# Kernel tuning notes

Hardware: AMD Instinct MI355X
Metric: run time of the kernel (lower is better)

Reference implementation:

```python
import jax, jax.numpy as jnp
import numpy as np

# Fixed supermask = [3, 4, 16, 28, 0, 0, 0, 3]:
#   preproc: relu(Linear x3); l1 = GCN(x); l2 = GCN(l1); l3 = GCN(l2);
#   out = relu(Linear z3((l1+l2+l3)/3))
HIDDEN = 64


def gcn_conv(h, W, b, src, dst, norm, n_nodes):
    # PyG GCNConv: h' = scatter_add(norm * (hW)[src] -> dst) + b
    hw = h @ W                                  # [N, F]
    msg = hw[src] * norm[:, None]               # gather + scale  [E+N, F]
    agg = jax.ops.segment_sum(msg, dst, num_segments=n_nodes)
    return agg + b


def setup_inputs() -> dict:
    key = jax.random.key(0)
    ks = jax.random.split(key, 12)
    N, E, NFEAT, NCLASS = 100000, 1000000, 256, 40
    x = jax.random.normal(ks[0], (N, NFEAT), dtype=jnp.float32)
    edge_index = jax.random.randint(ks[1], (2, E), 0, N, dtype=jnp.int64)
    s = 1.0 / np.sqrt(NFEAT)
    h = 1.0 / np.sqrt(HIDDEN)
    return {
        "x": x,
        "edge_index": edge_index,
        "Wx": jax.random.uniform(ks[2], (NFEAT, HIDDEN), jnp.float32, -s, s),
        "bx": jnp.zeros((HIDDEN,), jnp.float32),
        "W1": jax.random.uniform(ks[3], (HIDDEN, HIDDEN), jnp.float32, -h, h),
        "b1": jnp.zeros((HIDDEN,), jnp.float32),
        "W2": jax.random.uniform(ks[4], (HIDDEN, HIDDEN), jnp.float32, -h, h),
        "b2": jnp.zeros((HIDDEN,), jnp.float32),
        "W3": jax.random.uniform(ks[5], (HIDDEN, HIDDEN), jnp.float32, -h, h),
        "b3": jnp.zeros((HIDDEN,), jnp.float32),
        "Wz": jax.random.uniform(ks[6], (HIDDEN, NCLASS), jnp.float32, -h, h),
        "bz": jnp.zeros((NCLASS,), jnp.float32),
    }


def reference(x, edge_index, Wx, bx, W1, b1, W2, b2, W3, b3, Wz, bz):
    n = x.shape[0]
    # add self-loops (PyG GCNConv default)
    loop = jnp.arange(n, dtype=edge_index.dtype)
    src = jnp.concatenate([edge_index[0], loop])
    dst = jnp.concatenate([edge_index[1], loop])
    deg = jax.ops.segment_sum(jnp.ones_like(dst, dtype=x.dtype), dst, num_segments=n)
    dinv = jnp.where(deg > 0, jax.lax.rsqrt(deg), 0.0)
    norm = dinv[src] * dinv[dst]                 # [E+N]

    h0 = jax.nn.relu(x @ Wx + bx)                # x_3(relu) o x3(Linear)
    l1 = gcn_conv(h0, W1, b1, src, dst, norm, n)
    l2 = gcn_conv(l1, W2, b2, src, dst, norm, n)
    l3 = gcn_conv(l2, W3, b3, src, dst, norm, n)
    z = (l1 + l2 + l3) / 3.0
    return jax.nn.relu(z @ Wz + bz)
```

## Files before the change

kernel.cpp:

```cpp
#include <hip/hip_runtime.h>

#define NFEAT 256
#define HID 64
#define NCLASS 40
#define EPB 4096
#define BCAP 8192

typedef _Float16 half8 __attribute__((ext_vector_type(8)));
typedef float floatx4 __attribute__((ext_vector_type(4)));

struct BinSM {
    int lcnt[256], loff[256], lcur[256], gbase[256], sc[256];
    int sdst[EPB];
    int words[EPB];
};

__global__ __launch_bounds__(256) void k_pre(const int* __restrict__ src, const int* __restrict__ dst,
                                             int* __restrict__ bcur, int* __restrict__ bwords,
                                             int nbuckets, int E, int nbin,
                                             const float* __restrict__ W1, const float* __restrict__ W2,
                                             const float* __restrict__ W3, _Float16* __restrict__ Wt16,
                                             const float* __restrict__ x, const float* __restrict__ Wx,
                                             const float* __restrict__ bx, _Float16* __restrict__ h0,
                                             int N, int ngemm) {
    __shared__ __align__(16) char smraw[sizeof(BinSM)];
    int t = threadIdx.x;
    int bid = blockIdx.x;

    if (bid >= nbin && bid < nbin + 3) {
        int l = bid - nbin;
        const float* Ws = (l == 0) ? W1 : (l == 1) ? W2 : W3;
        _Float16* wt = Wt16 + l * 4096;
        for (int i = t; i < 4096; i += 256) {
            int col = i >> 6, k = i & 63;
            wt[i] = (_Float16)Ws[k * HID + col];
        }
        return;
    }

    if (bid >= nbin + 3) {
        _Float16 (*Wt)[264] = (_Float16 (*)[264])smraw;
        {
            int c = t & 63, k0 = (t >> 6) * 64;
            for (int k = k0; k < k0 + 64; ++k)
                Wt[c][k] = (_Float16)Wx[k * HID + c];
        }
        __syncthreads();
        int lane = t & 63, wv = t >> 6;
        int lg = lane >> 4, ln = lane & 15;
        int gb = bid - nbin - 3;
        int wid = gb * 4 + wv;
        int nw = ngemm * 4;
        float bb[4];
        #pragma unroll
        for (int g = 0; g < 4; ++g) bb[g] = bx[g * 16 + ln];
        int ntiles = N >> 4;
        for (int tile = wid; tile < ntiles; tile += nw) {
            int row0 = tile << 4;
            const float* xr = x + (size_t)(row0 + ln) * NFEAT + lg * 8;
            float4 av[16];
            #pragma unroll
            for (int ks = 0; ks < 8; ++ks) {
                av[2 * ks]     = *(const float4*)(xr + ks * 32);
                av[2 * ks + 1] = *(const float4*)(xr + ks * 32 + 4);
            }
            floatx4 acc[4] = {{0.f,0.f,0.f,0.f},{0.f,0.f,0.f,0.f},{0.f,0.f,0.f,0.f},{0.f,0.f,0.f,0.f}};
            #pragma unroll
            for (int ks = 0; ks < 8; ++ks) {
                float4 a0 = av[2 * ks], a1 = av[2 * ks + 1];
                half8 a;
                a[0]=(_Float16)a0.x; a[1]=(_Float16)a0.y; a[2]=(_Float16)a0.z; a[3]=(_Float16)a0.w;
                a[4]=(_Float16)a1.x; a[5]=(_Float16)a1.y; a[6]=(_Float16)a1.z; a[7]=(_Float16)a1.w;
                #pragma unroll
                for (int g = 0; g < 4; ++g) {
                    half8 b = *(const half8*)&Wt[g * 16 + ln][ks * 32 + lg * 8];
                    acc[g] = __builtin_amdgcn_mfma_f32_16x16x32_f16(a, b, acc[g], 0, 0, 0);
                }
            }
            #pragma unroll
            for (int g = 0; g < 4; ++g) {
                #pragma unroll
                for (int r = 0; r < 4; ++r) {
                    int row = row0 + lg * 4 + r;
                    h0[(size_t)row * HID + g * 16 + ln] = (_Float16)fmaxf(acc[g][r] + bb[g], 0.f);
                }
            }
        }
        return;
    }

    BinSM* sm = (BinSM*)smraw;
    int base = bid * EPB;
    int n = E - base; if (n > EPB) n = EPB;
    sm->lcnt[t] = 0;
    __syncthreads();
    for (int i = t; i < n; i += 256) {
        int d = dst[base + i];
        sm->sdst[i] = d;
        atomicAdd(&sm->lcnt[d >> 9], 1);
    }
    __syncthreads();
    int v = sm->lcnt[t];
    sm->sc[t] = v; __syncthreads();
    for (int o = 1; o < 256; o <<= 1) {
        int add = (t >= o) ? sm->sc[t - o] : 0;
        __syncthreads();
        sm->sc[t] += add;
        __syncthreads();
    }
    int excl = sm->sc[t] - v;
    sm->loff[t] = excl; sm->lcur[t] = excl;
    __syncthreads();
    for (int i = t; i < n; i += 256) {
        int d = sm->sdst[i], s = src[base + i];
        int b = d >> 9;
        int p = atomicAdd(&sm->lcur[b], 1);
        sm->words[p] = s | ((d & 511) << 17);
    }
    __syncthreads();
    if (t < nbuckets) {
        int c = sm->lcnt[t];
        sm->gbase[t] = c > 0 ? atomicAdd(&bcur[t], c) : 0;
    }
    __syncthreads();
    int lane = t & 63, wv = t >> 6;
    for (int b = wv; b < nbuckets; b += 4) {
        int o = sm->loff[b], c = sm->lcnt[b], gb = sm->gbase[b];
        int* dstp = bwords + (size_t)b * BCAP;
        for (int i = lane; i < c; i += 64) {
            int gp = gb + i;
            if (gp < BCAP) dstp[gp] = sm->words[o + i];
        }
    }
}

__global__ __launch_bounds__(256) void k_csr(const int* __restrict__ bcur, const int* __restrict__ bwords,
                                             int* __restrict__ csr, unsigned* __restrict__ pk,
                                             float* __restrict__ dinv, int N) {
    __shared__ int cnt[512], cur[512], sc[256];
    __shared__ int lcsr[BCAP];
    int t = threadIdx.x;
    int b = blockIdx.x;
    int nodebase = b << 9;
    int nb = bcur[b]; if (nb > BCAP) nb = BCAP;
    cnt[t] = 0; cnt[t + 256] = 0;
    __syncthreads();
    const int* wp = bwords + (size_t)b * BCAP;
    for (int i = t; i < nb; i += 256)
        atomicAdd(&cnt[wp[i] >> 17], 1);
    __syncthreads();
    int v0 = cnt[2 * t], v1 = cnt[2 * t + 1];
    int p = v0 + v1;
    sc[t] = p; __syncthreads();
    for (int o = 1; o < 256; o <<= 1) {
        int add = (t >= o) ? sc[t - o] : 0;
        __syncthreads();
        sc[t] += add;
        __syncthreads();
    }
    int e = sc[t] - p;
    cur[2 * t] = e; cur[2 * t + 1] = e + v0;
    #pragma unroll
    for (int j = 0; j < 2; ++j) {
        int node = nodebase + 2 * t + j;
        if (node < N) {
            int c = cnt[2 * t + j]; if (c > 2047) c = 2047;
            pk[node] = (unsigned)(b * BCAP + cur[2 * t + j]) | ((unsigned)c << 21);
            dinv[node] = rsqrtf((float)c + 1.0f);
        }
    }
    __syncthreads();
    for (int i = t; i < nb; i += 256) {
        int w = wp[i];
        int pos = atomicAdd(&cur[w >> 17], 1);
        lcsr[pos] = w & 0x1FFFF;
    }
    __syncthreads();
    int* cp = csr + (size_t)b * BCAP;
    for (int i = t; i < nb; i += 256) cp[i] = lcsr[i];
}

template<int WRN>
__global__ __launch_bounds__(256) void k_layer(const _Float16* __restrict__ Ph, const int* __restrict__ csr,
                                               const unsigned* __restrict__ pk, const float* __restrict__ dinv,
                                               const _Float16* __restrict__ Wt, const float* __restrict__ b,
                                               float* __restrict__ normf,
                                               _Float16* __restrict__ Lout, int N) {
    __shared__ _Float16 z[32][72];
    __shared__ _Float16 ot[32][72];
    int t = threadIdx.x;
    int lane = t & 63, wv = t >> 6;
    int sg = lane >> 3, f8 = lane & 7;
    int lg = lane >> 4, ln = lane & 15;
    int nb = blockIdx.x << 5;
    int node = nb + wv * 8 + sg;
    bool valid = node < N;
    int nodec = valid ? node : (N - 1);
    int col = wv * 16 + ln;
    half8 bf0 = *(const half8*)(Wt + col * 64 + lg * 8);
    half8 bf1 = *(const half8*)(Wt + col * 64 + 32 + lg * 8);
    float bb = b[col];

    unsigned pkv = valid ? pk[node] : 0u;
    int off = (int)(pkv & 0x1FFFFFu);
    int c = (int)(pkv >> 21);
    float dd = valid ? dinv[node] : 0.f;
    const _Float16* pb = Ph + f8 * 8;
    float acc[8];
    {
        half8 self = *(const half8*)(pb + (size_t)nodec * HID);
        float dd2 = dd * dd;
        #pragma unroll
        for (int j = 0; j < 8; ++j) acc[j] = (float)self[j] * dd2;
    }
    int ecur = f8;
    bool ok = ecur < c;
    int s_cur = ok ? csr[off + ecur] : nodec;
    float nm_cur;
    if (WRN) {
        nm_cur = ok ? dinv[s_cur] * dd : 0.f;
        if (ok) normf[off + ecur] = nm_cur;
    } else {
        nm_cur = ok ? normf[off + ecur] : 0.f;
    }
    for (int jj = 0; jj < c; jj += 8) {
        int en = jj + 8 + f8;
        bool okn = en < c;
        int s_nxt = okn ? csr[off + en] : nodec;
        float nm_nxt;
        if (WRN) {
            nm_nxt = okn ? dinv[s_nxt] * dd : 0.f;
            if (okn) normf[off + en] = nm_nxt;
        } else {
            nm_nxt = okn ? normf[off + en] : 0.f;
        }
        #pragma unroll
        for (int j = 0; j < 8; ++j) {
            int ss = __shfl(s_cur, j, 8);
            float nn = __shfl(nm_cur, j, 8);
            half8 v = *(const half8*)(pb + (size_t)ss * HID);
            #pragma unroll
            for (int q = 0; q < 8; ++q) acc[q] = fmaf((float)v[q], nn, acc[q]);
        }
        s_cur = s_nxt; nm_cur = nm_nxt;
    }
    {
        half8 zv;
        #pragma unroll
        for (int j = 0; j < 8; ++j) zv[j] = (_Float16)acc[j];
        *(half8*)&z[wv * 8 + sg][f8 * 8] = zv;
    }
    __syncthreads();
    floatx4 acc0 = {0.f, 0.f, 0.f, 0.f}, acc1 = {0.f, 0.f, 0.f, 0.f};
    {
        half8 a0 = *(const half8*)&z[ln][lg * 8];
        half8 a1 = *(const half8*)&z[16 + ln][lg * 8];
        acc0 = __builtin_amdgcn_mfma_f32_16x16x32_f16(a0, bf0, acc0, 0, 0, 0);
        acc1 = __builtin_amdgcn_mfma_f32_16x16x32_f16(a1, bf0, acc1, 0, 0, 0);
        a0 = *(const half8*)&z[ln][32 + lg * 8];
        a1 = *(const half8*)&z[16 + ln][32 + lg * 8];
        acc0 = __builtin_amdgcn_mfma_f32_16x16x32_f16(a0, bf1, acc0, 0, 0, 0);
        acc1 = __builtin_amdgcn_mfma_f32_16x16x32_f16(a1, bf1, acc1, 0, 0, 0);
    }
    #pragma unroll
    for (int r = 0; r < 4; ++r) {
        ot[lg * 4 + r][wv * 16 + ln] = (_Float16)(acc0[r] + bb);
        ot[16 + lg * 4 + r][wv * 16 + ln] = (_Float16)(acc1[r] + bb);
    }
    __syncthreads();
    {
        int row = t >> 3, c8 = t & 7;
        int onode = nb + row;
        if (onode < N)
            *(half8*)(Lout + (size_t)onode * HID + c8 * 8) = *(const half8*)&ot[row][c8 * 8];
    }
}

__global__ __launch_bounds__(256) void k_gemm_out(const _Float16* __restrict__ L1, const _Float16* __restrict__ L2,
                                                  const _Float16* __restrict__ L3, const float* __restrict__ Wz,
                                                  const float* __restrict__ bz, float* __restrict__ outp, int N) {
    int t = threadIdx.x;
    int lane = t & 63, lg = lane >> 4, ln = lane & 15;
    int wid = (blockIdx.x * 256 + t) >> 6;
    int nw = (gridDim.x * 256) >> 6;
    half8 b[2][3];
    float bb[3];
    #pragma unroll
    for (int g = 0; g < 3; ++g) {
        int col = g * 16 + ln;
        bb[g] = (col < NCLASS) ? bz[col] : 0.f;
        #pragma unroll
        for (int ks = 0; ks < 2; ++ks)
            #pragma unroll
            for (int j = 0; j < 8; ++j)
                b[ks][g][j] = (col < NCLASS) ? (_Float16)(Wz[(ks * 32 + lg * 8 + j) * NCLASS + col] * (1.f / 3.f)) : (_Float16)0.f;
    }
    int ntiles = N >> 4;
    for (int tile = wid; tile < ntiles; tile += nw) {
        int row0 = tile << 4;
        size_t rb = (size_t)(row0 + ln) * HID + lg * 8;
        floatx4 acc[3] = {{0.f,0.f,0.f,0.f},{0.f,0.f,0.f,0.f},{0.f,0.f,0.f,0.f}};
        #pragma unroll
        for (int ks = 0; ks < 2; ++ks) {
            half8 a1 = *(const half8*)(L1 + rb + ks * 32);
            half8 a2 = *(const half8*)(L2 + rb + ks * 32);
            half8 a3 = *(const half8*)(L3 + rb + ks * 32);
            half8 a;
            #pragma unroll
            for (int j = 0; j < 8; ++j)
                a[j] = (_Float16)((float)a1[j] + (float)a2[j] + (float)a3[j]);
            #pragma unroll
            for (int g = 0; g < 3; ++g)
                acc[g] = __builtin_amdgcn_mfma_f32_16x16x32_f16(a, b[ks][g], acc[g], 0, 0, 0);
        }
        #pragma unroll
        for (int g = 0; g < 3; ++g) {
            int col = g * 16 + ln;
            if (col < NCLASS) {
                #pragma unroll
                for (int r = 0; r < 4; ++r)
                    outp[(size_t)(row0 + lg * 4 + r) * NCLASS + col] = fmaxf(acc[g][r] + bb[g], 0.f);
            }
        }
    }
}

extern "C" void kernel_launch(void* const* d_in, const int* in_sizes, int n_in,
                              void* d_out, int out_size, void* d_ws, size_t ws_size,
                              hipStream_t stream) {
    const float* x  = (const float*)d_in[0];
    const int*   ei = (const int*)d_in[1];
    const float* Wx = (const float*)d_in[2];
    const float* bx = (const float*)d_in[3];
    const float* W1 = (const float*)d_in[4];
    const float* b1 = (const float*)d_in[5];
    const float* W2 = (const float*)d_in[6];
    const float* b2 = (const float*)d_in[7];
    const float* W3 = (const float*)d_in[8];
    const float* b3 = (const float*)d_in[9];
    const float* Wz = (const float*)d_in[10];
    const float* bz = (const float*)d_in[11];
    float* out = (float*)d_out;

    int N = in_sizes[0] / NFEAT;
    int E = in_sizes[1] / 2;
    const int* src = ei;
    const int* dst = ei + E;
    int nbuckets = (N + 511) >> 9;

    size_t nh = (size_t)N * HID;
    size_t Npad = ((size_t)N + 7) / 8 * 8;
    int*      bcur = (int*)d_ws;
    float*    dinv = (float*)d_ws + 256;
    unsigned* pk   = (unsigned*)(dinv + Npad);
    _Float16* H0   = (_Float16*)(pk + Npad);
    _Float16* L1   = H0 + nh;
    _Float16* L2   = L1 + nh;
    _Float16* L3   = L2 + nh;
    int*      bwords = (int*)(L3 + nh);
    int*      csr  = bwords + (size_t)nbuckets * BCAP;
    _Float16* Wt16 = (_Float16*)(csr + (size_t)nbuckets * BCAP);
    float*    normf = (float*)(Wt16 + 3 * 4096);

    int nbin = (E + EPB - 1) / EPB;
    int ngemm = 512;
    hipMemsetAsync(bcur, 0, 256 * sizeof(int), stream);
    k_pre<<<nbin + 3 + ngemm, 256, 0, stream>>>(src, dst, bcur, bwords, nbuckets, E, nbin,
                                                W1, W2, W3, Wt16, x, Wx, bx, H0, N, ngemm);
    k_csr<<<nbuckets, 256, 0, stream>>>(bcur, bwords, csr, pk, dinv, N);

    int layer_blocks = (N + 31) / 32;
    k_layer<1><<<layer_blocks, 256, 0, stream>>>(H0, csr, pk, dinv, Wt16,          b1, normf, L1, N);
    k_layer<0><<<layer_blocks, 256, 0, stream>>>(L1, csr, pk, dinv, Wt16 + 4096,   b2, normf, L2, N);
    k_layer<0><<<layer_blocks, 256, 0, stream>>>(L2, csr, pk, dinv, Wt16 + 8192,   b3, normf, L3, N);

    k_gemm_out<<<512, 256, 0, stream>>>(L1, L2, L3, Wz, bz, out, N);
}
```

Baseline: 285.2 us.

## Move input GEMM into CSR kernel and use shuffle-based block scans

Moves the x@Wx+relu preprocessing GEMM out of the binning kernel and into a new 512-thread CSR-build kernel, so it runs alongside CSR construction rather than binning. The CSR kernel now handles one node per thread with 512 threads. Both kernels replace the shared-memory Hillis-Steele scan, which needed many __syncthreads, with a wave-shuffle scan. The aim is to balance the work across the two preprocessing kernels and cut barrier overhead. The trade-off is that the GEMM now waits until binning has finished, and the higher thread count per block may reduce occupancy.

```diff
diff --git a/kernel.cpp b/kernel.cpp
--- a/kernel.cpp
+++ b/kernel.cpp
@@ -9,8 +9,34 @@
 typedef _Float16 half8 __attribute__((ext_vector_type(8)));
 typedef float floatx4 __attribute__((ext_vector_type(4)));
 
+__device__ __forceinline__ int wave_iscan(int v, int lane) {
+    #pragma unroll
+    for (int o = 1; o < 64; o <<= 1) {
+        int u = __shfl_up(v, o, 64);
+        if (lane >= o) v += u;
+    }
+    return v;
+}
+
+template<int NT>
+__device__ __forceinline__ int block_iscan(int v, int t, int* wsum) {
+    const int NW = NT / 64;
+    int lane = t & 63, wv = t >> 6;
+    int s = wave_iscan(v, lane);
+    if (lane == 63) wsum[wv] = s;
+    __syncthreads();
+    if (wv == 0) {
+        int w = (lane < NW) ? wsum[lane] : 0;
+        int ws = wave_iscan(w, lane);
+        if (lane < NW) wsum[lane] = ws;
+    }
+    __syncthreads();
+    int add = (wv > 0) ? wsum[wv - 1] : 0;
+    return s + add;
+}
+
 struct BinSM {
-    int lcnt[256], loff[256], lcur[256], gbase[256], sc[256];
+    int lcnt[256], loff[256], lcur[256], gbase[256], wsum[4];
     int sdst[EPB];
     int words[EPB];
 };
@@ -19,15 +45,12 @@
                                              int* __restrict__ bcur, int* __restrict__ bwords,
                                              int nbuckets, int E, int nbin,
                                              const float* __restrict__ W1, const float* __restrict__ W2,
-                                             const float* __restrict__ W3, _Float16* __restrict__ Wt16,
-                                             const float* __restrict__ x, const float* __restrict__ Wx,
-                                             const float* __restrict__ bx, _Float16* __restrict__ h0,
-                                             int N, int ngemm) {
+                                             const float* __restrict__ W3, _Float16* __restrict__ Wt16) {
     __shared__ __align__(16) char smraw[sizeof(BinSM)];
     int t = threadIdx.x;
     int bid = blockIdx.x;
 
-    if (bid >= nbin && bid < nbin + 3) {
+    if (bid >= nbin) {
         int l = bid - nbin;
         const float* Ws = (l == 0) ? W1 : (l == 1) ? W2 : W3;
         _Float16* wt = Wt16 + l * 4096;
@@ -38,19 +61,71 @@
         return;
     }
 
-    if (bid >= nbin + 3) {
+    BinSM* sm = (BinSM*)smraw;
+    int base = bid * EPB;
+    int n = E - base; if (n > EPB) n = EPB;
+    sm->lcnt[t] = 0;
+    __syncthreads();
+    for (int i = t; i < n; i += 256) {
+        int d = dst[base + i];
+        sm->sdst[i] = d;
+        atomicAdd(&sm->lcnt[d >> 9], 1);
+    }
+    __syncthreads();
+    int v = sm->lcnt[t];
+    int incl = block_iscan<256>(v, t, sm->wsum);
+    int excl = incl - v;
+    sm->loff[t] = excl; sm->lcur[t] = excl;
+    __syncthreads();
+    for (int i = t; i < n; i += 256) {
+        int d = sm->sdst[i], s = src[base + i];
+        int b = d >> 9;
+        int p = atomicAdd(&sm->lcur[b], 1);
+        sm->words[p] = s | ((d & 511) << 17);
+    }
+    __syncthreads();
+    if (t < nbuckets) {
+        int c = sm->lcnt[t];
+        sm->gbase[t] = c > 0 ? atomicAdd(&bcur[t], c) : 0;
+    }
+    __syncthreads();
+    int lane = t & 63, wv = t >> 6;
+    for (int b = wv; b < nbuckets; b += 4) {
+        int o = sm->loff[b], c = sm->lcnt[b], gb = sm->gbase[b];
+        int* dstp = bwords + (size_t)b * BCAP;
+        for (int i = lane; i < c; i += 64) {
+            int gp = gb + i;
+            if (gp < BCAP) dstp[gp] = sm->words[o + i];
+        }
+    }
+}
+
+struct CsrSM {
+    int cnt[512], cur[512], wsum[8];
+    int lcsr[BCAP];
+};
+
+__global__ __launch_bounds__(512) void k_csr2(const int* __restrict__ bcur, const int* __restrict__ bwords,
+                                              int* __restrict__ csr, unsigned* __restrict__ pk,
+                                              float* __restrict__ dinv, int N, int ncsr,
+                                              const float* __restrict__ x, const float* __restrict__ Wx,
+                                              const float* __restrict__ bx, _Float16* __restrict__ h0,
+                                              int ngemm) {
+    __shared__ __align__(16) char smraw[sizeof(CsrSM)];
+    int t = threadIdx.x;
+    int bid = blockIdx.x;
+
+    if (bid >= ncsr) {
         _Float16 (*Wt)[264] = (_Float16 (*)[264])smraw;
         {
-            int c = t & 63, k0 = (t >> 6) * 64;
-            for (int k = k0; k < k0 + 64; ++k)
+            int c = t & 63, k0 = (t >> 6) * 32;
+            for (int k = k0; k < k0 + 32; ++k)
                 Wt[c][k] = (_Float16)Wx[k * HID + c];
         }
         __syncthreads();
-        int lane = t & 63, wv = t >> 6;
-        int lg = lane >> 4, ln = lane & 15;
-        int gb = bid - nbin - 3;
-        int wid = gb * 4 + wv;
-        int nw = ngemm * 4;
+        int lane = t & 63, lg = lane >> 4, ln = lane & 15;
+        int wid = ((bid - ncsr) * 512 + t) >> 6;
+        int nw = ngemm * 8;
         float bb[4];
         #pragma unroll
         for (int g = 0; g < 4; ++g) bb[g] = bx[g * 16 + ln];
@@ -89,95 +164,35 @@
         return;
     }
 
-    BinSM* sm = (BinSM*)smraw;
-    int base = bid * EPB;
-    int n = E - base; if (n > EPB) n = EPB;
-    sm->lcnt[t] = 0;
-    __syncthreads();
-    for (int i = t; i < n; i += 256) {
-        int d = dst[base + i];
-        sm->sdst[i] = d;
-        atomicAdd(&sm->lcnt[d >> 9], 1);
-    }
-    __syncthreads();
-    int v = sm->lcnt[t];
-    sm->sc[t] = v; __syncthreads();
-    for (int o = 1; o < 256; o <<= 1) {
-        int add = (t >= o) ? sm->sc[t - o] : 0;
-        __syncthreads();
-        sm->sc[t] += add;
-        __syncthreads();
-    }
-    int excl = sm->sc[t] - v;
-    sm->loff[t] = excl; sm->lcur[t] = excl;
-    __syncthreads();
-    for (int i = t; i < n; i += 256) {
-        int d = sm->sdst[i], s = src[base + i];
-        int b = d >> 9;
-        int p = atomicAdd(&sm->lcur[b], 1);
-        sm->words[p] = s | ((d & 511) << 17);
-    }
-    __syncthreads();
-    if (t < nbuckets) {
-        int c = sm->lcnt[t];
-        sm->gbase[t] = c > 0 ? atomicAdd(&bcur[t], c) : 0;
-    }
-    __syncthreads();
-    int lane = t & 63, wv = t >> 6;
-    for (int b = wv; b < nbuckets; b += 4) {
-        int o = sm->loff[b], c = sm->lcnt[b], gb = sm->gbase[b];
-        int* dstp = bwords + (size_t)b * BCAP;
-        for (int i = lane; i < c; i += 64) {
-            int gp = gb + i;
-            if (gp < BCAP) dstp[gp] = sm->words[o + i];
-        }
-    }
-}
-
-__global__ __launch_bounds__(256) void k_csr(const int* __restrict__ bcur, const int* __restrict__ bwords,
-                                             int* __restrict__ csr, unsigned* __restrict__ pk,
-                                             float* __restrict__ dinv, int N) {
-    __shared__ int cnt[512], cur[512], sc[256];
-    __shared__ int lcsr[BCAP];
-    int t = threadIdx.x;
-    int b = blockIdx.x;
+    CsrSM* sm = (CsrSM*)smraw;
+    int b = bid;
     int nodebase = b << 9;
     int nb = bcur[b]; if (nb > BCAP) nb = BCAP;
-    cnt[t] = 0; cnt[t + 256] = 0;
+    sm->cnt[t] = 0;
     __syncthreads();
     const int* wp = bwords + (size_t)b * BCAP;
-    for (int i = t; i < nb; i += 256)
-        atomicAdd(&cnt[wp[i] >> 17], 1);
-    __syncthreads();
-    int v0 = cnt[2 * t], v1 = cnt[2 * t + 1];
-    int p = v0 + v1;
-    sc[t] = p; __syncthreads();
-    for (int o = 1; o < 256; o <<= 1) {
-        int add = (t >= o) ? sc[t - o] : 0;
-        __syncthreads();
-        sc[t] += add;
-        __syncthreads();
-    }
-    int e = sc[t] - p;
-    cur[2 * t] = e; cur[2 * t + 1] = e + v0;
-    #pragma unroll
-    for (int j = 0; j < 2; ++j) {
-        int node = nodebase + 2 * t + j;
-        if (node < N) {
-            int c = cnt[2 * t + j]; if (c > 2047) c = 2047;
-            pk[node] = (unsigned)(b * BCAP + cur[2 * t + j]) | ((unsigned)c << 21);
-            dinv[node] = rsqrtf((float)c + 1.0f);
-        }
-    }
-    __syncthreads();
-    for (int i = t; i < nb; i += 256) {
+    for (int i = t; i < nb; i += 512)
+        atomicAdd(&sm->cnt[wp[i] >> 17], 1);
+    __syncthreads();
+    int v = sm->cnt[t];
+    int incl = block_iscan<512>(v, t, sm->wsum);
+    int excl = incl - v;
+    sm->cur[t] = excl;
+    int node = nodebase + t;
+    if (node < N) {
+        int c = v > 2047 ? 2047 : v;
+        pk[node] = (unsigned)(b * BCAP + excl) | ((unsigned)c << 21);
+        dinv[node] = rsqrtf((float)c + 1.0f);
+    }
+    __syncthreads();
+    for (int i = t; i < nb; i += 512) {
         int w = wp[i];
-        int pos = atomicAdd(&cur[w >> 17], 1);
-        lcsr[pos] = w & 0x1FFFF;
+        int pos = atomicAdd(&sm->cur[w >> 17], 1);
+        sm->lcsr[pos] = w & 0x1FFFF;
     }
     __syncthreads();
     int* cp = csr + (size_t)b * BCAP;
-    for (int i = t; i < nb; i += 256) cp[i] = lcsr[i];
+    for (int i = t; i < nb; i += 512) cp[i] = sm->lcsr[i];
 }
 
 template<int WRN>
@@ -363,11 +378,11 @@
     float*    normf = (float*)(Wt16 + 3 * 4096);
 
     int nbin = (E + EPB - 1) / EPB;
-    int ngemm = 512;
+    int ngemm = 256;
     hipMemsetAsync(bcur, 0, 256 * sizeof(int), stream);
-    k_pre<<<nbin + 3 + ngemm, 256, 0, stream>>>(src, dst, bcur, bwords, nbuckets, E, nbin,
-                                                W1, W2, W3, Wt16, x, Wx, bx, H0, N, ngemm);
-    k_csr<<<nbuckets, 256, 0, stream>>>(bcur, bwords, csr, pk, dinv, N);
+    k_pre<<<nbin + 3, 256, 0, stream>>>(src, dst, bcur, bwords, nbuckets, E, nbin, W1, W2, W3, Wt16);
+    k_csr2<<<nbuckets + ngemm, 512, 0, stream>>>(bcur, bwords, csr, pk, dinv, N, nbuckets,
+                                                 x, Wx, bx, H0, ngemm);
 
     int layer_blocks = (N + 31) / 32;
     k_layer<1><<<layer_blocks, 256, 0, stream>>>(H0, csr, pk, dinv, Wt16,          b1, normf, L1, N);
```

Result: slower. 296.2 us (+3.9%).

## Degree-sort nodes per bucket, fuse output GEMM into last layer, wave-shuffle scans

Applied to the files above, without the earlier changes.

Replaces the shared-memory Hillis-Steele scans with wave-shuffle block scans. k_csr now builds a per-bucket node order sorted by degree class, and the layer kernels process nodes in that order so that waves handle nodes with similar edge counts and diverge less. The final output GEMM is fused into the third layer kernel, which removes a launch and the L3 write and re-read. The cost is an indirection through the order array, scattered output writes, and padded order slots for the last bucket, which rely on unfilled entries being treated as invalid nodes.

```diff
diff --git a/kernel.cpp b/kernel.cpp
--- a/kernel.cpp
+++ b/kernel.cpp
@@ -9,8 +9,38 @@
 typedef _Float16 half8 __attribute__((ext_vector_type(8)));
 typedef float floatx4 __attribute__((ext_vector_type(4)));
 
+__device__ __forceinline__ int wave_iscan(int v, int lane) {
+    #pragma unroll
+    for (int o = 1; o < 64; o <<= 1) {
+        int u = __shfl_up(v, o, 64);
+        if (lane >= o) v += u;
+    }
+    return v;
+}
+
+template<int NT>
+__device__ __forceinline__ int block_iscan(int v, int t, int* wsum) {
+    const int NW = NT / 64;
+    int lane = t & 63, wv = t >> 6;
+    int s = wave_iscan(v, lane);
+    if (lane == 63) wsum[wv] = s;
+    __syncthreads();
+    if (wv == 0) {
+        int w = (lane < NW) ? wsum[lane] : 0;
+        #pragma unroll
+        for (int o = 1; o < NW; o <<= 1) {
+            int u = __shfl_up(w, o, 64);
+            if (lane >= o) w += u;
+        }
+        if (lane < NW) wsum[lane] = w;
+    }
+    __syncthreads();
+    int add = (wv > 0) ? wsum[wv - 1] : 0;
+    return s + add;
+}
+
 struct BinSM {
-    int lcnt[256], loff[256], lcur[256], gbase[256], sc[256];
+    int lcnt[256], loff[256], lcur[256], gbase[256], wsum[4];
     int sdst[EPB];
     int words[EPB];
 };
@@ -101,14 +131,8 @@
     }
     __syncthreads();
     int v = sm->lcnt[t];
-    sm->sc[t] = v; __syncthreads();
-    for (int o = 1; o < 256; o <<= 1) {
-        int add = (t >= o) ? sm->sc[t - o] : 0;
-        __syncthreads();
-        sm->sc[t] += add;
-        __syncthreads();
-    }
-    int excl = sm->sc[t] - v;
+    int incl = block_iscan<256>(v, t, sm->wsum);
+    int excl = incl - v;
     sm->loff[t] = excl; sm->lcur[t] = excl;
     __syncthreads();
     for (int i = t; i < n; i += 256) {
@@ -136,14 +160,16 @@
 
 __global__ __launch_bounds__(256) void k_csr(const int* __restrict__ bcur, const int* __restrict__ bwords,
                                              int* __restrict__ csr, unsigned* __restrict__ pk,
-                                             float* __restrict__ dinv, int N) {
-    __shared__ int cnt[512], cur[512], sc[256];
+                                             float* __restrict__ dinv, int* __restrict__ order, int N) {
+    __shared__ int cnt[512], cur[512], wsum[4];
+    __shared__ int hist[32], hcur[32];
     __shared__ int lcsr[BCAP];
     int t = threadIdx.x;
     int b = blockIdx.x;
     int nodebase = b << 9;
     int nb = bcur[b]; if (nb > BCAP) nb = BCAP;
     cnt[t] = 0; cnt[t + 256] = 0;
+    if (t < 32) hist[t] = 0;
     __syncthreads();
     const int* wp = bwords + (size_t)b * BCAP;
     for (int i = t; i < nb; i += 256)
@@ -151,15 +177,13 @@
     __syncthreads();
     int v0 = cnt[2 * t], v1 = cnt[2 * t + 1];
     int p = v0 + v1;
-    sc[t] = p; __syncthreads();
-    for (int o = 1; o < 256; o <<= 1) {
-        int add = (t >= o) ? sc[t - o] : 0;
-        __syncthreads();
-        sc[t] += add;
-        __syncthreads();
-    }
-    int e = sc[t] - p;
+    int incl = block_iscan<256>(p, t, wsum);
+    int e = incl - p;
     cur[2 * t] = e; cur[2 * t + 1] = e + v0;
+    int kc0 = (v0 + 7) >> 3; if (kc0 > 31) kc0 = 31;
+    int kc1 = (v1 + 7) >> 3; if (kc1 > 31) kc1 = 31;
+    atomicAdd(&hist[kc0], 1);
+    atomicAdd(&hist[kc1], 1);
     #pragma unroll
     for (int j = 0; j < 2; ++j) {
         int node = nodebase + 2 * t + j;
@@ -170,6 +194,23 @@
         }
     }
     __syncthreads();
+    if (t < 32) {
+        int h = hist[t];
+        int s = h;
+        #pragma unroll
+        for (int o = 1; o < 32; o <<= 1) {
+            int u = __shfl_up(s, o, 32);
+            if ((t & 31) >= o) s += u;
+        }
+        hcur[t] = s - h;
+    }
+    __syncthreads();
+    {
+        int r0 = atomicAdd(&hcur[kc0], 1);
+        int r1 = atomicAdd(&hcur[kc1], 1);
+        order[(b << 9) + r0] = nodebase + 2 * t;
+        order[(b << 9) + r1] = nodebase + 2 * t + 1;
+    }
     for (int i = t; i < nb; i += 256) {
         int w = wp[i];
         int pos = atomicAdd(&cur[w >> 17], 1);
@@ -180,22 +221,26 @@
     for (int i = t; i < nb; i += 256) cp[i] = lcsr[i];
 }
 
-template<int WRN>
+template<int WRN, int FUSE>
 __global__ __launch_bounds__(256) void k_layer(const _Float16* __restrict__ Ph, const int* __restrict__ csr,
                                                const unsigned* __restrict__ pk, const float* __restrict__ dinv,
                                                const _Float16* __restrict__ Wt, const float* __restrict__ b,
-                                               float* __restrict__ normf,
-                                               _Float16* __restrict__ Lout, int N) {
+                                               float* __restrict__ normf, const int* __restrict__ order,
+                                               _Float16* __restrict__ Lout, int N,
+                                               const _Float16* __restrict__ L1p, const _Float16* __restrict__ L2p,
+                                               const float* __restrict__ Wz, const float* __restrict__ bz,
+                                               float* __restrict__ outp) {
     __shared__ _Float16 z[32][72];
     __shared__ _Float16 ot[32][72];
+    __shared__ float oout[32][48];
     int t = threadIdx.x;
     int lane = t & 63, wv = t >> 6;
     int sg = lane >> 3, f8 = lane & 7;
     int lg = lane >> 4, ln = lane & 15;
     int nb = blockIdx.x << 5;
-    int node = nb + wv * 8 + sg;
+    int node = order[nb + wv * 8 + sg];
     bool valid = node < N;
-    int nodec = valid ? node : (N - 1);
+    int nodec = valid ? node : 0;
     int col = wv * 16 + ln;
     half8 bf0 = *(const half8*)(Wt + col * 64 + lg * 8);
     half8 bf1 = *(const half8*)(Wt + col * 64 + 32 + lg * 8);
@@ -203,7 +248,7 @@
 
     unsigned pkv = valid ? pk[node] : 0u;
     int off = (int)(pkv & 0x1FFFFFu);
-    int c = (int)(pkv >> 21);
+    int c = valid ? (int)(pkv >> 21) : 0;
     float dd = valid ? dinv[node] : 0.f;
     const _Float16* pb = Ph + f8 * 8;
     float acc[8];
@@ -268,59 +313,58 @@
         ot[16 + lg * 4 + r][wv * 16 + ln] = (_Float16)(acc1[r] + bb);
     }
     __syncthreads();
-    {
+
+    if (!FUSE) {
         int row = t >> 3, c8 = t & 7;
-        int onode = nb + row;
+        int onode = order[nb + row];
         if (onode < N)
             *(half8*)(Lout + (size_t)onode * HID + c8 * 8) = *(const half8*)&ot[row][c8 * 8];
-    }
-}
-
-__global__ __launch_bounds__(256) void k_gemm_out(const _Float16* __restrict__ L1, const _Float16* __restrict__ L2,
-                                                  const _Float16* __restrict__ L3, const float* __restrict__ Wz,
-                                                  const float* __restrict__ bz, float* __restrict__ outp, int N) {
-    int t = threadIdx.x;
-    int lane = t & 63, lg = lane >> 4, ln = lane & 15;
-    int wid = (blockIdx.x * 256 + t) >> 6;
-    int nw = (gridDim.x * 256) >> 6;
-    half8 b[2][3];
-    float bb[3];
-    #pragma unroll
-    for (int g = 0; g < 3; ++g) {
-        int col = g * 16 + ln;
-        bb[g] = (col < NCLASS) ? bz[col] : 0.f;
-        #pragma unroll
-        for (int ks = 0; ks < 2; ++ks)
+    } else {
+        {
+            int row = t >> 3, c8 = t & 7;
+            int onode = order[nb + row];
+            half8 a1, a2;
+            if (onode < N) {
+                a1 = *(const half8*)(L1p + (size_t)onode * HID + c8 * 8);
+                a2 = *(const half8*)(L2p + (size_t)onode * HID + c8 * 8);
+            } else {
+                #pragma unroll
+                for (int j = 0; j < 8; ++j) { a1[j] = (_Float16)0.f; a2[j] = (_Float16)0.f; }
+            }
+            half8 l3 = *(const half8*)&ot[row][c8 * 8];
+            half8 s;
             #pragma unroll
             for (int j = 0; j < 8; ++j)
-                b[ks][g][j] = (col < NCLASS) ? (_Float16)(Wz[(ks * 32 + lg * 8 + j) * NCLASS + col] * (1.f / 3.f)) : (_Float16)0.f;
-    }
-    int ntiles = N >> 4;
-    for (int tile = wid; tile < ntiles; tile += nw) {
-        int row0 = tile << 4;
-        size_t rb = (size_t)(row0 + ln) * HID + lg * 8;
-        floatx4 acc[3] = {{0.f,0.f,0.f,0.f},{0.f,0.f,0.f,0.f},{0.f,0.f,0.f,0.f}};
-        #pragma unroll
-        for (int ks = 0; ks < 2; ++ks) {
-            half8 a1 = *(const half8*)(L1 + rb + ks * 32);
-            half8 a2 = *(const half8*)(L2 + rb + ks * 32);
-            half8 a3 = *(const half8*)(L3 + rb + ks * 32);
-            half8 a;
-            #pragma unroll
-            for (int j = 0; j < 8; ++j)
-                a[j] = (_Float16)((float)a1[j] + (float)a2[j] + (float)a3[j]);
-            #pragma unroll
-            for (int g = 0; g < 3; ++g)
-                acc[g] = __builtin_amdgcn_mfma_f32_16x16x32_f16(a, b[ks][g], acc[g], 0, 0, 0);
-        }
-        #pragma unroll
-        for (int g = 0; g < 3; ++g) {
-            int col = g * 16 + ln;
-            if (col < NCLASS) {
-                #pragma unroll
-                for (int r = 0; r < 4; ++r)
-                    outp[(size_t)(row0 + lg * 4 + r) * NCLASS + col] = fmaxf(acc[g][r] + bb[g], 0.f);
+                s[j] = (_Float16)(((float)a1[j] + (float)a2[j] + (float)l3[j]) * (1.f / 3.f));
+            *(half8*)&z[row][c8 * 8] = s;
+        }
+        __syncthreads();
+        for (int tk = wv; tk < 6; tk += 4) {
+            int rt = tk / 3, cg = tk % 3;
+            int ocol = cg * 16 + ln;
+            bool okc = ocol < NCLASS;
+            half8 bw0, bw1;
+            #pragma unroll
+            for (int j = 0; j < 8; ++j) {
+                bw0[j] = okc ? (_Float16)Wz[(lg * 8 + j) * NCLASS + ocol] : (_Float16)0.f;
+                bw1[j] = okc ? (_Float16)Wz[(32 + lg * 8 + j) * NCLASS + ocol] : (_Float16)0.f;
             }
+            float bbz = okc ? bz[ocol] : 0.f;
+            floatx4 ac = {0.f, 0.f, 0.f, 0.f};
+            half8 a0 = *(const half8*)&z[rt * 16 + ln][lg * 8];
+            ac = __builtin_amdgcn_mfma_f32_16x16x32_f16(a0, bw0, ac, 0, 0, 0);
+            a0 = *(const half8*)&z[rt * 16 + ln][32 + lg * 8];
+            ac = __builtin_amdgcn_mfma_f32_16x16x32_f16(a0, bw1, ac, 0, 0, 0);
+            #pragma unroll
+            for (int r = 0; r < 4; ++r)
+                oout[rt * 16 + lg * 4 + r][cg * 16 + ln] = fmaxf(ac[r] + bbz, 0.f);
+        }
+        __syncthreads();
+        for (int i = t; i < 32 * NCLASS; i += 256) {
+            int row = i / NCLASS, ocol = i % NCLASS;
+            int onode = order[nb + row];
+            if (onode < N)
+                outp[(size_t)onode * NCLASS + ocol] = oout[row][ocol];
         }
     }
 }
@@ -361,18 +405,20 @@
     int*      csr  = bwords + (size_t)nbuckets * BCAP;
     _Float16* Wt16 = (_Float16*)(csr + (size_t)nbuckets * BCAP);
     float*    normf = (float*)(Wt16 + 3 * 4096);
+    int*      order = (int*)(normf + (size_t)nbuckets * BCAP);
 
     int nbin = (E + EPB - 1) / EPB;
     int ngemm = 512;
     hipMemsetAsync(bcur, 0, 256 * sizeof(int), stream);
     k_pre<<<nbin + 3 + ngemm, 256, 0, stream>>>(src, dst, bcur, bwords, nbuckets, E, nbin,
                                                 W1, W2, W3, Wt16, x, Wx, bx, H0, N, ngemm);
-    k_csr<<<nbuckets, 256, 0, stream>>>(bcur, bwords, csr, pk, dinv, N);
-
-    int layer_blocks = (N + 31) / 32;
-    k_layer<1><<<layer_blocks, 256, 0, stream>>>(H0, csr, pk, dinv, Wt16,          b1, normf, L1, N);
-    k_layer<0><<<layer_blocks, 256, 0, stream>>>(L1, csr, pk, dinv, Wt16 + 4096,   b2, normf, L2, N);
-    k_layer<0><<<layer_blocks, 256, 0, stream>>>(L2, csr, pk, dinv, Wt16 + 8192,   b3, normf, L3, N);
-
-    k_gemm_out<<<512, 256, 0, stream>>>(L1, L2, L3, Wz, bz, out, N);
-}
+    k_csr<<<nbuckets, 256, 0, stream>>>(bcur, bwords, csr, pk, dinv, order, N);
+
+    int layer_blocks = nbuckets * 16;
+    k_layer<1,0><<<layer_blocks, 256, 0, stream>>>(H0, csr, pk, dinv, Wt16,        b1, normf, order, L1, N,
+                                                   nullptr, nullptr, nullptr, nullptr, nullptr);
+    k_layer<0,0><<<layer_blocks, 256, 0, stream>>>(L1, csr, pk, dinv, Wt16 + 4096, b2, normf, order, L2, N,
+                                                   nullptr, nullptr, nullptr, nullptr, nullptr);
+    k_layer<0,1><<<layer_blocks, 256, 0, stream>>>(L2, csr, pk, dinv, Wt16 + 8192, b3, normf, order, L3, N,
+                                                   L1, L2, Wz, bz, out);
+}
```

New measurement: 314.7 us. 10.3% more time.
